# Kernel tuning notes

Measured on AMD Instinct MI355X. Metric: run time of the kernel, lower is better.

Reference implementation:

```python
import jax, jax.numpy as jnp
import numpy as np

EPS = 1e-12  # F.normalize eps

def _l2norm(v, axis):
    n = jnp.sqrt(jnp.sum(v * v, axis=axis, keepdims=True))
    return v / jnp.maximum(n, EPS)

def setup_inputs() -> dict:
    key = jax.random.key(0)
    ks = jax.random.split(key, 4)
    B, N, C, centers = 128, 196, 768, 64
    x = jax.random.normal(ks[0], (B, N, C), dtype=jnp.float32)
    k_c = jax.random.normal(ks[1], (C, centers), dtype=jnp.float32)
    v_c = jax.random.normal(ks[2], (centers, N, N), dtype=jnp.float32)
    proj_w = jax.random.normal(ks[3], (C, C), dtype=jnp.float32) * (C ** -0.5)
    proj_b = jnp.zeros((C,), dtype=jnp.float32)
    return {"x": x, "k_c": k_c, "v_c": v_c, "proj_w": proj_w, "proj_b": proj_b}

def reference(x, k_c, v_c, proj_w, proj_b):
    # x: (B, N, C); k_c: (C, centers); v_c: (centers, N, N)
    C = x.shape[-1]
    scale = C ** -0.5
    q = x.mean(axis=1)                                  # (B, C)
    attn = _l2norm(q, -1) @ _l2norm(k_c, 0)             # (B, centers)
    attn = jax.nn.softmax(attn * scale, axis=-1)        # (B, centers)
    # attention-weighted mixture of basis matrices: (B,centers)x(centers,N*N) GEMM
    v = jnp.einsum('bc,cnm->bnm', attn, v_c)            # (B, N, N)
    out = jnp.einsum('bnm,bmd->bnd', v, x)              # (B, N, C)
    out = out @ proj_w.T + proj_b                        # Linear(dim, dim)
    return out
```

## Files before the change

kernel.cpp:

```cpp
#include <hip/hip_runtime.h>
#include <hip/hip_bf16.h>


#define NB   128
#define NN   196
#define NC   768
#define NCEN 64
#define RPAD 256
#define KPAD 224
#define BGRP 32
#define QPARTS 7

using bf16x8 = __attribute__((ext_vector_type(8))) short;
using f32x4  = __attribute__((ext_vector_type(4))) float;

__device__ __forceinline__ void async_copy16(const void* g, void* l) {
    __builtin_amdgcn_global_load_lds((const __attribute__((address_space(1))) void*)g,
                                     (__attribute__((address_space(3))) void*)l, 16, 0, 0);
}

__global__ __launch_bounds__(192)
void convert_x_kernel(const float* __restrict__ x, __hip_bfloat16* __restrict__ x_bf,
                      float* __restrict__ q_part) {
    __shared__ float qsh[NC];
    int b = blockIdx.x, y = blockIdx.y, t = threadIdx.x;
    int cg = t % 96, rg = t / 96;
    int c = cg * 8;
    const float* xp = x + (size_t)b * NN * NC + c;
    __hip_bfloat16* xo = x_bf + (size_t)b * RPAD * NC + c;
    float s[8] = {0.f, 0.f, 0.f, 0.f, 0.f, 0.f, 0.f, 0.f};
    int m0 = y * 28 + rg * 14;
#pragma unroll 2
    for (int m = m0; m < m0 + 14; ++m) {
        const float* src = xp + (size_t)m * NC;
        float4 v0 = *(const float4*)src;
        float4 v1 = *(const float4*)(src + 4);
        union { bf16x8 v; __hip_bfloat16 h[8]; } u;
        u.h[0] = __float2bfloat16(v0.x); s[0] += v0.x;
        u.h[1] = __float2bfloat16(v0.y); s[1] += v0.y;
        u.h[2] = __float2bfloat16(v0.z); s[2] += v0.z;
        u.h[3] = __float2bfloat16(v0.w); s[3] += v0.w;
        u.h[4] = __float2bfloat16(v1.x); s[4] += v1.x;
        u.h[5] = __float2bfloat16(v1.y); s[5] += v1.y;
        u.h[6] = __float2bfloat16(v1.z); s[6] += v1.z;
        u.h[7] = __float2bfloat16(v1.w); s[7] += v1.w;
        *(bf16x8*)(xo + (size_t)m * NC) = u.v;
    }
    if (y == 6) {
        bf16x8 z = {};
        int mz0 = 196 + rg * 14;
        for (int m = mz0; m < mz0 + 14; ++m)
            *(bf16x8*)(xo + (size_t)m * NC) = z;
    }
    if (rg == 0) {
#pragma unroll
        for (int j = 0; j < 8; ++j) qsh[c + j] = s[j];
    }
    __syncthreads();
    if (rg == 1) {
        float* qp = q_part + ((size_t)y * NB + b) * NC + c;
        float4 o0 = make_float4(qsh[c] + s[0], qsh[c + 1] + s[1],
                                qsh[c + 2] + s[2], qsh[c + 3] + s[3]);
        float4 o1 = make_float4(qsh[c + 4] + s[4], qsh[c + 5] + s[5],
                                qsh[c + 6] + s[6], qsh[c + 7] + s[7]);
        *(float4*)qp = o0;
        *(float4*)(qp + 4) = o1;
    }
}

__global__ __launch_bounds__(256)
void convert_w_kernel(const float* __restrict__ w, __hip_bfloat16* __restrict__ w_bf) {
    int i = (blockIdx.x * 256 + threadIdx.x) * 8;
    if (i >= NC * NC) return;
    float4 v0 = *(const float4*)(w + i);
    float4 v1 = *(const float4*)(w + i + 4);
    union { bf16x8 v; __hip_bfloat16 h[8]; } u;
    u.h[0] = __float2bfloat16(v0.x);
    u.h[1] = __float2bfloat16(v0.y);
    u.h[2] = __float2bfloat16(v0.z);
    u.h[3] = __float2bfloat16(v0.w);
    u.h[4] = __float2bfloat16(v1.x);
    u.h[5] = __float2bfloat16(v1.y);
    u.h[6] = __float2bfloat16(v1.z);
    u.h[7] = __float2bfloat16(v1.w);
    *(bf16x8*)(w_bf + i) = u.v;
}

__global__ __launch_bounds__(256)
void attn_kernel(const float* __restrict__ q_part, const float* __restrict__ k_c,
                 float* __restrict__ attn) {
    const float SCALE = 0.03608439182435161f;
    int b = blockIdx.x, t = threadIdx.x;
    __shared__ float qs[NC];
    __shared__ float red[256];
    __shared__ float pd[4][NCEN];
    __shared__ float pk[4][NCEN];

    const size_t PS = (size_t)NB * NC;
    for (int i = t; i < NC; i += 256) {
        size_t idx = (size_t)b * NC + i;
        float acc = 0.f;
#pragma unroll
        for (int p = 0; p < QPARTS; ++p) acc += q_part[p * PS + idx];
        qs[i] = acc * (1.0f / (float)NN);
    }
    __syncthreads();

    float s = 0.f;
    for (int i = t; i < NC; i += 256) { float v = qs[i]; s += v * v; }
    red[t] = s;
    __syncthreads();
    for (int o = 128; o > 0; o >>= 1) {
        if (t < o) red[t] += red[t + o];
        __syncthreads();
    }
    float qn = sqrtf(red[0]);

    int j = t & 63, part = t >> 6;
    float d = 0.f, kk = 0.f;
    int c0 = part * 192;
    for (int c = c0; c < c0 + 192; ++c) {
        float kv = k_c[c * NCEN + j];
        d += kv * qs[c];
        kk += kv * kv;
    }
    pd[part][j] = d;
    pk[part][j] = kk;
    __syncthreads();

    if (t < NCEN) {
        float dot = pd[0][t] + pd[1][t] + pd[2][t] + pd[3][t];
        float kn  = sqrtf(pk[0][t] + pk[1][t] + pk[2][t] + pk[3][t]);
        float lg = dot / (fmaxf(qn, 1e-12f) * fmaxf(kn, 1e-12f)) * SCALE;
        float mx = lg;
        for (int o = 32; o > 0; o >>= 1) mx = fmaxf(mx, __shfl_xor(mx, o, 64));
        float e = expf(lg - mx);
        float sum = e;
        for (int o = 32; o > 0; o >>= 1) sum += __shfl_xor(sum, o, 64);
        attn[b * NCEN + t] = e / sum;
    }
}

__global__ __launch_bounds__(256)
void mix_kernel(const float* __restrict__ attn, const float* __restrict__ v_c,
                __hip_bfloat16* __restrict__ v_pad) {
    int n = blockIdx.x;
    int g = blockIdx.y;
    int m = threadIdx.x;

    __shared__ float sattn[BGRP][NCEN];
    for (int i = threadIdx.x; i < BGRP * NCEN; i += 256)
        sattn[i >> 6][i & 63] = attn[(g * BGRP + (i >> 6)) * NCEN + (i & 63)];
    __syncthreads();

    if (m >= KPAD) return;
    __hip_bfloat16 z = __float2bfloat16(0.f);
    size_t base = (size_t)n * KPAD + m;
    if (n >= NN || m >= NN) {
#pragma unroll
        for (int bb = 0; bb < BGRP; ++bb)
            v_pad[(size_t)(g * BGRP + bb) * RPAD * KPAD + base] = z;
        return;
    }
    float vc[NCEN];
    const float* vp = v_c + (size_t)n * NN + m;
#pragma unroll
    for (int c = 0; c < NCEN; ++c) vc[c] = vp[(size_t)c * NN * NN];
#pragma unroll
    for (int bb = 0; bb < BGRP; ++bb) {
        float acc = 0.f;
#pragma unroll
        for (int c = 0; c < NCEN; ++c) acc += sattn[bb][c] * vc[c];
        v_pad[(size_t)(g * BGRP + bb) * RPAD * KPAD + base] = __float2bfloat16(acc);
    }
}

template <int BK, bool OUT_BF16, int NBM, int NBN>
__global__ __launch_bounds__(256)
void gemm_nt(const __hip_bfloat16* __restrict__ A, size_t strideA,
             const __hip_bfloat16* __restrict__ Bm, size_t strideB,
             void* __restrict__ Cout, size_t strideC,
             const float* __restrict__ bias,
             int lda, int ldb, int ldc, int K, int Mstore, int Nstore) {
    constexpr int MPG = NBM * NBN;
    int L = blockIdx.x;
    int xcd = L & 7;
    int r = L >> 3;
    int q = r / MPG;
    int i5 = r - q * MPG;
    int bb = xcd + 8 * q;
    int bm = i5 % NBM;
    int bn = i5 / NBM;

    const unsigned short* Ab = (const unsigned short*)A + (size_t)bb * strideA + (size_t)bm * 128 * lda;
    const unsigned short* Bb = (const unsigned short*)Bm + (size_t)bb * strideB + (size_t)bn * 128 * ldb;

    __shared__ __align__(16) unsigned short sA[128 * BK];
    __shared__ __align__(16) unsigned short sB[128 * BK];

    int tid = threadIdx.x;
    int wave = tid >> 6, lane = tid & 63;
    int wr = wave >> 1, wc = wave & 1;
    int lrow = lane & 15, quad = lane >> 4;

    constexpr int CH  = BK / 8;
    constexpr int RPI = 64 / CH;
    constexpr int NI  = 32 / RPI;
    int srow = lane / CH;
    int sc   = lane % CH;
    int lc   = (BK == 64) ? (sc ^ (srow & 7)) : sc;

    const unsigned short* ga[NI];
    const unsigned short* gb[NI];
    unsigned short* la[NI];
    unsigned short* lb[NI];
#pragma unroll
    for (int i = 0; i < NI; ++i) {
        int row = wave * 32 + i * RPI + srow;
        ga[i] = Ab + (size_t)row * lda + lc * 8;
        gb[i] = Bb + (size_t)row * ldb + lc * 8;
        la[i] = &sA[(wave * 32 + i * RPI) * BK];
        lb[i] = &sB[(wave * 32 + i * RPI) * BK];
    }

    f32x4 acc[4][4] = {};

    for (int k0 = 0; k0 < K; k0 += BK) {
        __syncthreads();
#pragma unroll
        for (int i = 0; i < NI; ++i) async_copy16(ga[i] + k0, la[i]);
#pragma unroll
        for (int i = 0; i < NI; ++i) async_copy16(gb[i] + k0, lb[i]);
        __syncthreads();

#pragma unroll
        for (int kh = 0; kh < BK / 32; ++kh) {
            int pcbase = (BK == 64) ? ((kh * 4 + quad) ^ (lrow & 7)) : quad;
            bf16x8 af[4], bfr[4];
#pragma unroll
            for (int i = 0; i < 4; ++i)
                af[i] = *(const bf16x8*)(&sA[(wr * 64 + i * 16 + lrow) * BK + pcbase * 8]);
#pragma unroll
            for (int j = 0; j < 4; ++j)
                bfr[j] = *(const bf16x8*)(&sB[(wc * 64 + j * 16 + lrow) * BK + pcbase * 8]);
#pragma unroll
            for (int i = 0; i < 4; ++i)
#pragma unroll
                for (int j = 0; j < 4; ++j)
                    acc[i][j] = __builtin_amdgcn_mfma_f32_16x16x32_bf16(af[i], bfr[j], acc[i][j], 0, 0, 0);
        }
    }

    size_t cbase = (size_t)bb * strideC;
#pragma unroll
    for (int i = 0; i < 4; ++i) {
        int row0 = bm * 128 + wr * 64 + i * 16 + quad * 4;
#pragma unroll
        for (int j = 0; j < 4; ++j) {
            int col = bn * 128 + wc * 64 + j * 16 + lrow;
            if (col < Nstore) {
                float badd = bias ? bias[col] : 0.f;
#pragma unroll
                for (int r2 = 0; r2 < 4; ++r2) {
                    int row = row0 + r2;
                    if (row < Mstore) {
                        float v = acc[i][j][r2] + badd;
                        if (OUT_BF16)
                            ((__hip_bfloat16*)Cout)[cbase + (size_t)row * ldc + col] = __float2bfloat16(v);
                        else
                            ((float*)Cout)[cbase + (size_t)row * ldc + col] = v;
                    }
                }
            }
        }
    }
}

extern "C" void kernel_launch(void* const* d_in, const int* in_sizes, int n_in,
                              void* d_out, int out_size, void* d_ws, size_t ws_size,
                              hipStream_t stream) {
    const float* x      = (const float*)d_in[0];
    const float* k_c    = (const float*)d_in[1];
    const float* v_c    = (const float*)d_in[2];
    const float* proj_w = (const float*)d_in[3];
    const float* proj_b = (const float*)d_in[4];
    float* out = (float*)d_out;

    char* ws = (char*)d_ws;
    size_t off = 0;
    auto alloc = [&](size_t bytes) {
        void* p = ws + off;
        off = (off + bytes + 255) & ~(size_t)255;
        return p;
    };
    __hip_bfloat16* x_bf  = (__hip_bfloat16*)alloc((size_t)NB * RPAD * NC * 2);
    __hip_bfloat16* w_bf  = (__hip_bfloat16*)alloc((size_t)NC * NC * 2);
    __hip_bfloat16* xp_t  = (__hip_bfloat16*)alloc((size_t)NB * NC * KPAD * 2);
    __hip_bfloat16* v_pad = (__hip_bfloat16*)alloc((size_t)NB * RPAD * KPAD * 2);
    float* q_part = (float*)alloc((size_t)QPARTS * NB * NC * 4);
    float* attn   = (float*)alloc((size_t)NB * NCEN * 4);

    convert_x_kernel<<<dim3(NB, 7), 192, 0, stream>>>(x, x_bf, q_part);
    convert_w_kernel<<<dim3((NC * NC / 8 + 255) / 256), 256, 0, stream>>>(proj_w, w_bf);
    attn_kernel<<<dim3(NB), 256, 0, stream>>>(q_part, k_c, attn);
    mix_kernel<<<dim3(RPAD, NB / BGRP), 256, 0, stream>>>(attn, v_c, v_pad);

    gemm_nt<64, true, 6, 2><<<dim3(6 * 2 * NB), 256, 0, stream>>>(
        w_bf, 0, x_bf, (size_t)RPAD * NC, xp_t, (size_t)NC * KPAD, nullptr,
        NC, NC, KPAD, NC, NC, KPAD);

    gemm_nt<32, false, 2, 6><<<dim3(2 * 6 * NB), 256, 0, stream>>>(
        v_pad, (size_t)RPAD * KPAD, xp_t, (size_t)NC * KPAD, out, (size_t)NN * NC, proj_b,
        KPAD, KPAD, NC, KPAD, NN, NC);
}
```

Measured before the change: 289.1 us.

## Replace batched GEMMs with 256x256-tile, 8-wave, 4-stage pipelined MFMA kernel

Both batched bf16 GEMMs now use a new kernel with 256x256 output tiles, 512 threads (8 waves) and a 4-slot LDS ring fed by async global-to-LDS loads three K-steps ahead. It uses explicit vmcnt waits, split barriers and setprio around the MFMA bursts. K padding grows from 224 to 256 so the second GEMM runs a whole number of 32-wide K steps, with matching zero-fill changes in the convert and mix kernels. This targets per-iteration sync stalls and low reuse in the old 128x128 tiles, at the cost of more padded work in the second GEMM and heavy register and LDS use (128 KB LDS per block).

```diff
diff --git a/kernel.cpp b/kernel.cpp
--- a/kernel.cpp
+++ b/kernel.cpp
@@ -7,7 +7,7 @@
 #define NC   768
 #define NCEN 64
 #define RPAD 256
-#define KPAD 224
+#define KPAD 256
 #define BGRP 32
 #define QPARTS 7
 
@@ -48,8 +48,8 @@
     }
     if (y == 6) {
         bf16x8 z = {};
-        int mz0 = 196 + rg * 14;
-        for (int m = mz0; m < mz0 + 14; ++m)
+        int mz0 = 196 + rg * 30;
+        for (int m = mz0; m < mz0 + 30; ++m)
             *(bf16x8*)(xo + (size_t)m * NC) = z;
     }
     if (rg == 0) {
@@ -153,7 +153,6 @@
         sattn[i >> 6][i & 63] = attn[(g * BGRP + (i >> 6)) * NCEN + (i & 63)];
     __syncthreads();
 
-    if (m >= KPAD) return;
     __hip_bfloat16 z = __float2bfloat16(0.f);
     size_t base = (size_t)n * KPAD + m;
     if (n >= NN || m >= NN) {
@@ -175,101 +174,139 @@
     }
 }
 
-template <int BK, bool OUT_BF16, int NBM, int NBN>
-__global__ __launch_bounds__(256)
-void gemm_nt(const __hip_bfloat16* __restrict__ A, size_t strideA,
-             const __hip_bfloat16* __restrict__ Bm, size_t strideB,
-             void* __restrict__ Cout, size_t strideC,
-             const float* __restrict__ bias,
-             int lda, int ldb, int ldc, int K, int Mstore, int Nstore) {
-    constexpr int MPG = NBM * NBN;
+
+template <int SLOT, bool STG, int VMN>
+__device__ __forceinline__ void kstep(unsigned short* ldsw, int t,
+                                      const unsigned short* gA0, const unsigned short* gA1,
+                                      const unsigned short* gB0, const unsigned short* gB1,
+                                      int aW0, int aW1, int aR, int bR,
+                                      f32x4 (&acc)[8][4]) {
+    constexpr int S3 = (SLOT + 3) & 3;
+    __builtin_amdgcn_sched_barrier(0);
+    if constexpr (STG) {
+        size_t ko = (size_t)(t + 3) * 32;
+        async_copy16(gA0 + ko, ldsw + S3 * 8192 + aW0);
+        async_copy16(gA1 + ko, ldsw + S3 * 8192 + aW1);
+    }
+    bf16x8 af[4], bfr[4];
+#pragma unroll
+    for (int n = 0; n < 4; ++n)
+        bfr[n] = *(const bf16x8*)(ldsw + 32768 + SLOT * 8192 + bR + n * 512);
+#pragma unroll
+    for (int m = 0; m < 4; ++m)
+        af[m] = *(const bf16x8*)(ldsw + SLOT * 8192 + aR + m * 512);
+    __builtin_amdgcn_sched_barrier(0);
+    __builtin_amdgcn_s_barrier();
+    __builtin_amdgcn_s_setprio(1);
+#pragma unroll
+    for (int m = 0; m < 4; ++m)
+#pragma unroll
+        for (int n = 0; n < 4; ++n)
+            acc[m][n] = __builtin_amdgcn_mfma_f32_16x16x32_bf16(af[m], bfr[n], acc[m][n], 0, 0, 0);
+    __builtin_amdgcn_s_setprio(0);
+    __builtin_amdgcn_sched_barrier(0);
+    __builtin_amdgcn_s_barrier();
+    if constexpr (STG) {
+        size_t ko = (size_t)(t + 3) * 32;
+        async_copy16(gB0 + ko, ldsw + 32768 + S3 * 8192 + aW0);
+        async_copy16(gB1 + ko, ldsw + 32768 + S3 * 8192 + aW1);
+    }
+#pragma unroll
+    for (int m = 0; m < 4; ++m)
+        af[m] = *(const bf16x8*)(ldsw + SLOT * 8192 + aR + (4 + m) * 512);
+    __builtin_amdgcn_sched_barrier(0);
+    __builtin_amdgcn_s_barrier();
+    __builtin_amdgcn_s_setprio(1);
+#pragma unroll
+    for (int m = 0; m < 4; ++m)
+#pragma unroll
+        for (int n = 0; n < 4; ++n)
+            acc[4 + m][n] = __builtin_amdgcn_mfma_f32_16x16x32_bf16(af[m], bfr[n], acc[4 + m][n], 0, 0, 0);
+    __builtin_amdgcn_s_setprio(0);
+    __builtin_amdgcn_sched_barrier(0);
+    if constexpr (VMN >= 0)
+        asm volatile("s_waitcnt vmcnt(%0)" :: "i"(VMN) : "memory");
+    __builtin_amdgcn_s_barrier();
+    asm volatile("" ::: "memory");
+}
+
+template <int TK, bool OUT_BF16, bool TILE_N>
+__global__ __launch_bounds__(512, 2)
+void gemm_nt8(const __hip_bfloat16* __restrict__ A, size_t strideA,
+              const __hip_bfloat16* __restrict__ Bm, size_t strideB,
+              void* __restrict__ Cout, size_t strideC,
+              const float* __restrict__ bias,
+              int lda, int ldb, int ldc, int Mstore) {
+    __shared__ __align__(16) unsigned short ldsw[65536];
+
     int L = blockIdx.x;
-    int xcd = L & 7;
-    int r = L >> 3;
-    int q = r / MPG;
-    int i5 = r - q * MPG;
-    int bb = xcd + 8 * q;
-    int bm = i5 % NBM;
-    int bn = i5 / NBM;
-
-    const unsigned short* Ab = (const unsigned short*)A + (size_t)bb * strideA + (size_t)bm * 128 * lda;
-    const unsigned short* Bb = (const unsigned short*)Bm + (size_t)bb * strideB + (size_t)bn * 128 * ldb;
-
-    __shared__ __align__(16) unsigned short sA[128 * BK];
-    __shared__ __align__(16) unsigned short sB[128 * BK];
+    int w = (L & 7) * ((int)gridDim.x >> 3) + (L >> 3);
+    int bb = w / 3, tile = w - bb * 3;
+    int bm = TILE_N ? 0 : tile, bn = TILE_N ? tile : 0;
+
+    const unsigned short* Ab = (const unsigned short*)A + (size_t)bb * strideA + (size_t)(bm * 256) * lda;
+    const unsigned short* Bb = (const unsigned short*)Bm + (size_t)bb * strideB + (size_t)(bn * 256) * ldb;
 
     int tid = threadIdx.x;
-    int wave = tid >> 6, lane = tid & 63;
-    int wr = wave >> 1, wc = wave & 1;
+    int wid = tid >> 6, lane = tid & 63;
     int lrow = lane & 15, quad = lane >> 4;
-
-    constexpr int CH  = BK / 8;
-    constexpr int RPI = 64 / CH;
-    constexpr int NI  = 32 / RPI;
-    int srow = lane / CH;
-    int sc   = lane % CH;
-    int lc   = (BK == 64) ? (sc ^ (srow & 7)) : sc;
-
-    const unsigned short* ga[NI];
-    const unsigned short* gb[NI];
-    unsigned short* la[NI];
-    unsigned short* lb[NI];
-#pragma unroll
-    for (int i = 0; i < NI; ++i) {
-        int row = wave * 32 + i * RPI + srow;
-        ga[i] = Ab + (size_t)row * lda + lc * 8;
-        gb[i] = Bb + (size_t)row * ldb + lc * 8;
-        la[i] = &sA[(wave * 32 + i * RPI) * BK];
-        lb[i] = &sB[(wave * 32 + i * RPI) * BK];
-    }
-
-    f32x4 acc[4][4] = {};
-
-    for (int k0 = 0; k0 < K; k0 += BK) {
-        __syncthreads();
-#pragma unroll
-        for (int i = 0; i < NI; ++i) async_copy16(ga[i] + k0, la[i]);
-#pragma unroll
-        for (int i = 0; i < NI; ++i) async_copy16(gb[i] + k0, lb[i]);
-        __syncthreads();
-
-#pragma unroll
-        for (int kh = 0; kh < BK / 32; ++kh) {
-            int pcbase = (BK == 64) ? ((kh * 4 + quad) ^ (lrow & 7)) : quad;
-            bf16x8 af[4], bfr[4];
-#pragma unroll
-            for (int i = 0; i < 4; ++i)
-                af[i] = *(const bf16x8*)(&sA[(wr * 64 + i * 16 + lrow) * BK + pcbase * 8]);
-#pragma unroll
-            for (int j = 0; j < 4; ++j)
-                bfr[j] = *(const bf16x8*)(&sB[(wc * 64 + j * 16 + lrow) * BK + pcbase * 8]);
-#pragma unroll
-            for (int i = 0; i < 4; ++i)
-#pragma unroll
-                for (int j = 0; j < 4; ++j)
-                    acc[i][j] = __builtin_amdgcn_mfma_f32_16x16x32_bf16(af[i], bfr[j], acc[i][j], 0, 0, 0);
-        }
-    }
+    int wr = wid >> 2, wcn = wid & 3;
+
+    int srow = lane >> 2;
+    int sch = 8 * ((lane & 3) ^ ((lane >> 4) & 3));
+    const unsigned short* gA0 = Ab + (size_t)(16 * wid + srow) * lda + sch;
+    const unsigned short* gA1 = Ab + (size_t)(128 + 16 * wid + srow) * lda + sch;
+    const unsigned short* gB0 = Bb + (size_t)(16 * wid + srow) * ldb + sch;
+    const unsigned short* gB1 = Bb + (size_t)(128 + 16 * wid + srow) * ldb + sch;
+    int aW0 = wid * 512;
+    int aW1 = 4096 + wid * 512;
+
+    int rsw = 8 * (quad ^ (lrow >> 2));
+    int aR = (wr * 128 + lrow) * 32 + rsw;
+    int bR = (wcn * 64 + lrow) * 32 + rsw;
+
+    f32x4 acc[8][4] = {};
+
+#pragma unroll
+    for (int t = 0; t < 3; ++t) {
+        async_copy16(gA0 + t * 32, ldsw + t * 8192 + aW0);
+        async_copy16(gA1 + t * 32, ldsw + t * 8192 + aW1);
+        async_copy16(gB0 + t * 32, ldsw + 32768 + t * 8192 + aW0);
+        async_copy16(gB1 + t * 32, ldsw + 32768 + t * 8192 + aW1);
+    }
+    asm volatile("s_waitcnt vmcnt(8)" ::: "memory");
+    __builtin_amdgcn_s_barrier();
+    asm volatile("" ::: "memory");
+
+    for (int tb = 0; tb < TK / 4 - 1; ++tb) {
+        int t = tb * 4;
+        kstep<0, true, 8>(ldsw, t + 0, gA0, gA1, gB0, gB1, aW0, aW1, aR, bR, acc);
+        kstep<1, true, 8>(ldsw, t + 1, gA0, gA1, gB0, gB1, aW0, aW1, aR, bR, acc);
+        kstep<2, true, 8>(ldsw, t + 2, gA0, gA1, gB0, gB1, aW0, aW1, aR, bR, acc);
+        kstep<3, true, 8>(ldsw, t + 3, gA0, gA1, gB0, gB1, aW0, aW1, aR, bR, acc);
+    }
+    kstep<0, true,  8>(ldsw, TK - 4, gA0, gA1, gB0, gB1, aW0, aW1, aR, bR, acc);
+    kstep<1, false, 4>(ldsw, TK - 3, gA0, gA1, gB0, gB1, aW0, aW1, aR, bR, acc);
+    kstep<2, false, 0>(ldsw, TK - 2, gA0, gA1, gB0, gB1, aW0, aW1, aR, bR, acc);
+    kstep<3, false, -1>(ldsw, TK - 1, gA0, gA1, gB0, gB1, aW0, aW1, aR, bR, acc);
 
     size_t cbase = (size_t)bb * strideC;
 #pragma unroll
-    for (int i = 0; i < 4; ++i) {
-        int row0 = bm * 128 + wr * 64 + i * 16 + quad * 4;
-#pragma unroll
-        for (int j = 0; j < 4; ++j) {
-            int col = bn * 128 + wc * 64 + j * 16 + lrow;
-            if (col < Nstore) {
-                float badd = bias ? bias[col] : 0.f;
-#pragma unroll
-                for (int r2 = 0; r2 < 4; ++r2) {
-                    int row = row0 + r2;
-                    if (row < Mstore) {
-                        float v = acc[i][j][r2] + badd;
-                        if (OUT_BF16)
-                            ((__hip_bfloat16*)Cout)[cbase + (size_t)row * ldc + col] = __float2bfloat16(v);
-                        else
-                            ((float*)Cout)[cbase + (size_t)row * ldc + col] = v;
-                    }
+    for (int mrep = 0; mrep < 8; ++mrep) {
+        int row0 = bm * 256 + wr * 128 + mrep * 16 + quad * 4;
+#pragma unroll
+        for (int nrep = 0; nrep < 4; ++nrep) {
+            int col = bn * 256 + wcn * 64 + nrep * 16 + lrow;
+            float badd = bias ? bias[col] : 0.f;
+#pragma unroll
+            for (int r = 0; r < 4; ++r) {
+                int row = row0 + r;
+                if (row < Mstore) {
+                    float v = acc[mrep][nrep][r] + badd;
+                    if (OUT_BF16)
+                        ((__hip_bfloat16*)Cout)[cbase + (size_t)row * ldc + col] = __float2bfloat16(v);
+                    else
+                        ((float*)Cout)[cbase + (size_t)row * ldc + col] = v;
                 }
             }
         }
@@ -305,11 +342,11 @@
     attn_kernel<<<dim3(NB), 256, 0, stream>>>(q_part, k_c, attn);
     mix_kernel<<<dim3(RPAD, NB / BGRP), 256, 0, stream>>>(attn, v_c, v_pad);
 
-    gemm_nt<64, true, 6, 2><<<dim3(6 * 2 * NB), 256, 0, stream>>>(
+    gemm_nt8<24, true, false><<<dim3(3 * NB), 512, 0, stream>>>(
         w_bf, 0, x_bf, (size_t)RPAD * NC, xp_t, (size_t)NC * KPAD, nullptr,
-        NC, NC, KPAD, NC, NC, KPAD);
-
-    gemm_nt<32, false, 2, 6><<<dim3(2 * 6 * NB), 256, 0, stream>>>(
+        NC, NC, KPAD, NC);
+
+    gemm_nt8<8, false, true><<<dim3(3 * NB), 512, 0, stream>>>(
         v_pad, (size_t)RPAD * KPAD, xp_t, (size_t)NC * KPAD, out, (size_t)NN * NC, proj_b,
-        KPAD, KPAD, NC, KPAD, NN, NC);
-}
+        KPAD, KPAD, NC, NN);
+}
```

Result: slower. 315.1 us (+9.0%).

## Reorder GEMMs: mix x first, then project as one large flattened GEMM

Applied to the files above, without the earlier changes.

Changes the evaluation order from (V·(x·Wᵀ)) to ((V·x)·Wᵀ). The conversion kernel now writes x transposed into a padded bf16 layout through an LDS transpose and produces the column sums directly instead of partial sums. The batched V·x GEMM writes an intermediate of shape (B·224, C), and the projection runs as a single large GEMM over all batch rows with the weight shared, scattering valid rows to the output. The block-to-XCD mapping is also reworked. This aims to make the projection GEMM better shaped and to remove the reduction over partial sums, at the cost of extra padded rows in the flattened projection.

```diff
diff --git a/kernel.cpp b/kernel.cpp
--- a/kernel.cpp
+++ b/kernel.cpp
@@ -6,10 +6,9 @@
 #define NN   196
 #define NC   768
 #define NCEN 64
+#define MPAD 224
 #define RPAD 256
-#define KPAD 224
 #define BGRP 32
-#define QPARTS 7
 
 using bf16x8 = __attribute__((ext_vector_type(8))) short;
 using f32x4  = __attribute__((ext_vector_type(4))) float;
@@ -19,52 +18,58 @@
                                      (__attribute__((address_space(3))) void*)l, 16, 0, 0);
 }
 
-__global__ __launch_bounds__(192)
-void convert_x_kernel(const float* __restrict__ x, __hip_bfloat16* __restrict__ x_bf,
-                      float* __restrict__ q_part) {
-    __shared__ float qsh[NC];
-    int b = blockIdx.x, y = blockIdx.y, t = threadIdx.x;
-    int cg = t % 96, rg = t / 96;
-    int c = cg * 8;
-    const float* xp = x + (size_t)b * NN * NC + c;
-    __hip_bfloat16* xo = x_bf + (size_t)b * RPAD * NC + c;
-    float s[8] = {0.f, 0.f, 0.f, 0.f, 0.f, 0.f, 0.f, 0.f};
-    int m0 = y * 28 + rg * 14;
-#pragma unroll 2
-    for (int m = m0; m < m0 + 14; ++m) {
-        const float* src = xp + (size_t)m * NC;
-        float4 v0 = *(const float4*)src;
-        float4 v1 = *(const float4*)(src + 4);
+__global__ __launch_bounds__(256)
+void convert_x_kernel(const float* __restrict__ x, __hip_bfloat16* __restrict__ x_t,
+                      float* __restrict__ q_sum) {
+    __shared__ unsigned short lt[64 * 256];
+    __shared__ float qred[32][64];
+    int b = blockIdx.x, cc = blockIdx.y, t = threadIdx.x;
+    int c0 = cc * 64;
+    int c8 = t & 7;
+    int ms = t >> 3;
+    const float* xp = x + (size_t)b * NN * NC + c0 + c8 * 8;
+    float s[8] = {};
+#pragma unroll
+    for (int it = 0; it < 7; ++it) {
+        int m = ms + 32 * it;
         union { bf16x8 v; __hip_bfloat16 h[8]; } u;
-        u.h[0] = __float2bfloat16(v0.x); s[0] += v0.x;
-        u.h[1] = __float2bfloat16(v0.y); s[1] += v0.y;
-        u.h[2] = __float2bfloat16(v0.z); s[2] += v0.z;
-        u.h[3] = __float2bfloat16(v0.w); s[3] += v0.w;
-        u.h[4] = __float2bfloat16(v1.x); s[4] += v1.x;
-        u.h[5] = __float2bfloat16(v1.y); s[5] += v1.y;
-        u.h[6] = __float2bfloat16(v1.z); s[6] += v1.z;
-        u.h[7] = __float2bfloat16(v1.w); s[7] += v1.w;
-        *(bf16x8*)(xo + (size_t)m * NC) = u.v;
-    }
-    if (y == 6) {
-        bf16x8 z = {};
-        int mz0 = 196 + rg * 14;
-        for (int m = mz0; m < mz0 + 14; ++m)
-            *(bf16x8*)(xo + (size_t)m * NC) = z;
-    }
-    if (rg == 0) {
-#pragma unroll
-        for (int j = 0; j < 8; ++j) qsh[c + j] = s[j];
-    }
-    __syncthreads();
-    if (rg == 1) {
-        float* qp = q_part + ((size_t)y * NB + b) * NC + c;
-        float4 o0 = make_float4(qsh[c] + s[0], qsh[c + 1] + s[1],
-                                qsh[c + 2] + s[2], qsh[c + 3] + s[3]);
-        float4 o1 = make_float4(qsh[c + 4] + s[4], qsh[c + 5] + s[5],
-                                qsh[c + 6] + s[6], qsh[c + 7] + s[7]);
-        *(float4*)qp = o0;
-        *(float4*)(qp + 4) = o1;
+        u.v = (bf16x8){};
+        if (m < NN) {
+            float4 v0 = *(const float4*)(xp + (size_t)m * NC);
+            float4 v1 = *(const float4*)(xp + (size_t)m * NC + 4);
+            u.h[0] = __float2bfloat16(v0.x); s[0] += v0.x;
+            u.h[1] = __float2bfloat16(v0.y); s[1] += v0.y;
+            u.h[2] = __float2bfloat16(v0.z); s[2] += v0.z;
+            u.h[3] = __float2bfloat16(v0.w); s[3] += v0.w;
+            u.h[4] = __float2bfloat16(v1.x); s[4] += v1.x;
+            u.h[5] = __float2bfloat16(v1.y); s[5] += v1.y;
+            u.h[6] = __float2bfloat16(v1.z); s[6] += v1.z;
+            u.h[7] = __float2bfloat16(v1.w); s[7] += v1.w;
+        }
+        int msw = m ^ (c8 << 3);
+#pragma unroll
+        for (int j = 0; j < 8; ++j)
+            lt[(c8 * 8 + j) * 256 + msw] = ((unsigned short*)&u)[j];
+    }
+#pragma unroll
+    for (int j = 0; j < 8; ++j) qred[ms][c8 * 8 + j] = s[j];
+    __syncthreads();
+    {
+        int r = t >> 2, c4 = t & 3;
+        int key = (r >> 3) & 7;
+        __hip_bfloat16* xtr = x_t + (size_t)b * NC * MPAD + (size_t)(c0 + r) * MPAD;
+#pragma unroll
+        for (int ic = 0; ic < 7; ++ic) {
+            int ch = c4 + 4 * ic;
+            bf16x8 vv = *(const bf16x8*)&lt[r * 256 + ((ch ^ key) << 3)];
+            *(bf16x8*)(xtr + ch * 8) = vv;
+        }
+    }
+    if (t < 64) {
+        float q = 0.f;
+#pragma unroll
+        for (int ss = 0; ss < 32; ++ss) q += qred[ss][t];
+        q_sum[(size_t)b * NC + c0 + t] = q;
     }
 }
 
@@ -87,7 +92,7 @@
 }
 
 __global__ __launch_bounds__(256)
-void attn_kernel(const float* __restrict__ q_part, const float* __restrict__ k_c,
+void attn_kernel(const float* __restrict__ q_sum, const float* __restrict__ k_c,
                  float* __restrict__ attn) {
     const float SCALE = 0.03608439182435161f;
     int b = blockIdx.x, t = threadIdx.x;
@@ -96,14 +101,8 @@
     __shared__ float pd[4][NCEN];
     __shared__ float pk[4][NCEN];
 
-    const size_t PS = (size_t)NB * NC;
-    for (int i = t; i < NC; i += 256) {
-        size_t idx = (size_t)b * NC + i;
-        float acc = 0.f;
-#pragma unroll
-        for (int p = 0; p < QPARTS; ++p) acc += q_part[p * PS + idx];
-        qs[i] = acc * (1.0f / (float)NN);
-    }
+    for (int i = t; i < NC; i += 256)
+        qs[i] = q_sum[(size_t)b * NC + i] * (1.0f / (float)NN);
     __syncthreads();
 
     float s = 0.f;
@@ -153,13 +152,13 @@
         sattn[i >> 6][i & 63] = attn[(g * BGRP + (i >> 6)) * NCEN + (i & 63)];
     __syncthreads();
 
-    if (m >= KPAD) return;
+    if (m >= MPAD) return;
     __hip_bfloat16 z = __float2bfloat16(0.f);
-    size_t base = (size_t)n * KPAD + m;
+    size_t base = (size_t)n * MPAD + m;
     if (n >= NN || m >= NN) {
 #pragma unroll
         for (int bb = 0; bb < BGRP; ++bb)
-            v_pad[(size_t)(g * BGRP + bb) * RPAD * KPAD + base] = z;
+            v_pad[(size_t)(g * BGRP + bb) * RPAD * MPAD + base] = z;
         return;
     }
     float vc[NCEN];
@@ -171,26 +170,23 @@
         float acc = 0.f;
 #pragma unroll
         for (int c = 0; c < NCEN; ++c) acc += sattn[bb][c] * vc[c];
-        v_pad[(size_t)(g * BGRP + bb) * RPAD * KPAD + base] = __float2bfloat16(acc);
-    }
-}
-
-template <int BK, bool OUT_BF16, int NBM, int NBN>
+        v_pad[(size_t)(g * BGRP + bb) * RPAD * MPAD + base] = __float2bfloat16(acc);
+    }
+}
+
+template <int BK, int OUTMODE, int NBM, int NBN>
 __global__ __launch_bounds__(256)
 void gemm_nt(const __hip_bfloat16* __restrict__ A, size_t strideA,
              const __hip_bfloat16* __restrict__ Bm, size_t strideB,
              void* __restrict__ Cout, size_t strideC,
              const float* __restrict__ bias,
-             int lda, int ldb, int ldc, int K, int Mstore, int Nstore) {
+             int lda, int ldb, int ldc, int K, int Mstore) {
     constexpr int MPG = NBM * NBN;
     int L = blockIdx.x;
-    int xcd = L & 7;
-    int r = L >> 3;
-    int q = r / MPG;
-    int i5 = r - q * MPG;
-    int bb = xcd + 8 * q;
-    int bm = i5 % NBM;
-    int bn = i5 / NBM;
+    int w = (L & 7) * ((int)gridDim.x >> 3) + (L >> 3);
+    int bb = w / MPG;
+    int i5 = w - bb * MPG;
+    int bm = i5 / NBN, bn = i5 % NBN;
 
     const unsigned short* Ab = (const unsigned short*)A + (size_t)bb * strideA + (size_t)bm * 128 * lda;
     const unsigned short* Bb = (const unsigned short*)Bm + (size_t)bb * strideB + (size_t)bn * 128 * ldb;
@@ -258,17 +254,21 @@
 #pragma unroll
         for (int j = 0; j < 4; ++j) {
             int col = bn * 128 + wc * 64 + j * 16 + lrow;
-            if (col < Nstore) {
-                float badd = bias ? bias[col] : 0.f;
-#pragma unroll
-                for (int r2 = 0; r2 < 4; ++r2) {
-                    int row = row0 + r2;
+            float badd = (OUTMODE == 0 && bias) ? bias[col] : 0.f;
+#pragma unroll
+            for (int r2 = 0; r2 < 4; ++r2) {
+                int row = row0 + r2;
+                if (OUTMODE == 1) {
                     if (row < Mstore) {
-                        float v = acc[i][j][r2] + badd;
-                        if (OUT_BF16)
-                            ((__hip_bfloat16*)Cout)[cbase + (size_t)row * ldc + col] = __float2bfloat16(v);
-                        else
-                            ((float*)Cout)[cbase + (size_t)row * ldc + col] = v;
+                        ((__hip_bfloat16*)Cout)[cbase + (size_t)row * ldc + col] =
+                            __float2bfloat16(acc[i][j][r2]);
+                    }
+                } else {
+                    int b2 = row / MPAD;
+                    int n  = row - b2 * MPAD;
+                    if (n < NN) {
+                        ((float*)Cout)[((size_t)b2 * NN + n) * ldc + col] =
+                            acc[i][j][r2] + badd;
                     }
                 }
             }
@@ -293,23 +293,23 @@
         off = (off + bytes + 255) & ~(size_t)255;
         return p;
     };
-    __hip_bfloat16* x_bf  = (__hip_bfloat16*)alloc((size_t)NB * RPAD * NC * 2);
+    __hip_bfloat16* x_t   = (__hip_bfloat16*)alloc((size_t)NB * NC * MPAD * 2);
     __hip_bfloat16* w_bf  = (__hip_bfloat16*)alloc((size_t)NC * NC * 2);
-    __hip_bfloat16* xp_t  = (__hip_bfloat16*)alloc((size_t)NB * NC * KPAD * 2);
-    __hip_bfloat16* v_pad = (__hip_bfloat16*)alloc((size_t)NB * RPAD * KPAD * 2);
-    float* q_part = (float*)alloc((size_t)QPARTS * NB * NC * 4);
-    float* attn   = (float*)alloc((size_t)NB * NCEN * 4);
-
-    convert_x_kernel<<<dim3(NB, 7), 192, 0, stream>>>(x, x_bf, q_part);
+    __hip_bfloat16* tmp   = (__hip_bfloat16*)alloc((size_t)NB * MPAD * NC * 2);
+    __hip_bfloat16* v_pad = (__hip_bfloat16*)alloc((size_t)NB * RPAD * MPAD * 2);
+    float* q_sum = (float*)alloc((size_t)NB * NC * 4);
+    float* attn  = (float*)alloc((size_t)NB * NCEN * 4);
+
+    convert_x_kernel<<<dim3(NB, 12), 256, 0, stream>>>(x, x_t, q_sum);
     convert_w_kernel<<<dim3((NC * NC / 8 + 255) / 256), 256, 0, stream>>>(proj_w, w_bf);
-    attn_kernel<<<dim3(NB), 256, 0, stream>>>(q_part, k_c, attn);
+    attn_kernel<<<dim3(NB), 256, 0, stream>>>(q_sum, k_c, attn);
     mix_kernel<<<dim3(RPAD, NB / BGRP), 256, 0, stream>>>(attn, v_c, v_pad);
 
-    gemm_nt<64, true, 6, 2><<<dim3(6 * 2 * NB), 256, 0, stream>>>(
-        w_bf, 0, x_bf, (size_t)RPAD * NC, xp_t, (size_t)NC * KPAD, nullptr,
-        NC, NC, KPAD, NC, NC, KPAD);
-
-    gemm_nt<32, false, 2, 6><<<dim3(2 * 6 * NB), 256, 0, stream>>>(
-        v_pad, (size_t)RPAD * KPAD, xp_t, (size_t)NC * KPAD, out, (size_t)NN * NC, proj_b,
-        KPAD, KPAD, NC, KPAD, NN, NC);
-}
+    gemm_nt<32, 1, 2, 6><<<dim3(2 * 6 * NB), 256, 0, stream>>>(
+        v_pad, (size_t)RPAD * MPAD, x_t, (size_t)NC * MPAD, tmp, (size_t)MPAD * NC,
+        nullptr, MPAD, MPAD, NC, MPAD, MPAD);
+
+    gemm_nt<64, 0, 224, 6><<<dim3(224 * 6), 256, 0, stream>>>(
+        tmp, 0, w_bf, 0, out, 0,
+        proj_b, NC, NC, NC, NC, 224 * NB);
+}
```

New measurement: 329.9 us. 14.1% more time.
